# Kernel tuning notes

Hardware: AMD Instinct MI355X
Metric: run time of the kernel (lower is better)

## Reference

```python
import jax, jax.numpy as jnp
import numpy as np

MODEL_DIM = 1024
TOTAL_DIM = 1024
N_HEADS = 16
HEAD_DIM = TOTAL_DIM // N_HEADS


def setup_inputs() -> dict:
    key = jax.random.key(0)
    k1, k2, k3 = jax.random.split(key, 3)
    query = jax.random.normal(k1, (2, 2048, MODEL_DIM), dtype=jnp.float32)
    # nn.Linear(model_dim, 3*total_dim, bias=False): store as [in, out] for x @ W
    W_in = jax.random.normal(k2, (MODEL_DIM, 3 * TOTAL_DIM), dtype=jnp.float32) / np.sqrt(MODEL_DIM)
    W_out = jax.random.normal(k3, (TOTAL_DIM, MODEL_DIM), dtype=jnp.float32) / np.sqrt(TOTAL_DIM)
    return {"query": query, "W_in": W_in, "W_out": W_out}


def reference(query, W_in, W_out):
    B, S, _ = query.shape
    qkv = query @ W_in                      # [B, S, 3*D]
    q, k, v = jnp.split(qkv, 3, axis=-1)    # each [B, S, D]

    def to_heads(t):
        return t.reshape(B, S, N_HEADS, HEAD_DIM).transpose(0, 2, 1, 3)  # [B,H,S,d]

    q, k, v = to_heads(q), to_heads(k), to_heads(v)
    scale = 1.0 / np.sqrt(HEAD_DIM).astype(np.float32)
    scores = jnp.einsum('bhqd,bhkd->bhqk', q, k) * scale  # [B,H,S,S]
    causal = jnp.tril(jnp.ones((S, S), dtype=bool))
    scores = jnp.where(causal, scores, jnp.finfo(scores.dtype).min)
    probs = jax.nn.softmax(scores, axis=-1)
    attn = jnp.einsum('bhqk,bhkd->bhqd', probs, v)        # [B,H,S,d]
    attn = attn.transpose(0, 2, 1, 3).reshape(B, S, TOTAL_DIM)
    return attn @ W_out                     # [B, S, model_dim]
```

## Files before the change

### kernel.cpp

```cpp
#include <hip/hip_runtime.h>


typedef __bf16 bf16x8 __attribute__((ext_vector_type(8)));
typedef __bf16 bf16x4 __attribute__((ext_vector_type(4)));
typedef short s16x4 __attribute__((ext_vector_type(4)));
typedef float f32x4 __attribute__((ext_vector_type(4)));
typedef int i32x2 __attribute__((ext_vector_type(2)));

#define B_   2
#define S_   2048
#define DM   1024
#define NH   16
#define HD   64
#define N3   3072
#define M_   4096

#define SCALE_LOG2E 0.180336884f

__device__ __forceinline__ unsigned short f2bf(float f) {
  unsigned int u = __float_as_uint(f);
  u += 0x7fffu + ((u >> 16) & 1u);
  return (unsigned short)(u >> 16);
}

__device__ __forceinline__ void gload_lds16(void* lds, const void* g) {
  __builtin_amdgcn_global_load_lds(
      (__attribute__((address_space(1))) void*)g,
      (__attribute__((address_space(3))) void*)lds, 16, 0, 0);
}

__device__ __forceinline__ f32x4 mfma16(bf16x4 a, bf16x4 b, f32x4 c) {
#if __has_builtin(__builtin_amdgcn_mfma_f32_16x16x16_bf16)
  return __builtin_amdgcn_mfma_f32_16x16x16_bf16(a, b, c, 0, 0, 0);
#else
  return __builtin_amdgcn_mfma_f32_16x16x16bf16_1k(
      __builtin_bit_cast(s16x4, a), __builtin_bit_cast(s16x4, b), c, 0, 0, 0);
#endif
}

__device__ __forceinline__ int cvtpk(float s0, float s1) {
  int r;
  asm("v_cvt_pk_bf16_f32 %0, %1, %2" : "=v"(r) : "v"(s0), "v"(s1));
  return r;
}

__global__ __launch_bounds__(256) void prep(
    const float* __restrict__ query, const float* __restrict__ w_in,
    const float* __restrict__ w_out, unsigned short* __restrict__ qbf,
    unsigned short* __restrict__ w_in_t, unsigned short* __restrict__ w_out_t) {
  __shared__ float tile[32][33];
  const int bx = blockIdx.x;
  const int t = threadIdx.x;
  if (bx < 4096) {
    const int i = bx * 256 + t;
    const float4 v = ((const float4*)query)[i];
    ushort4 o;
    o.x = f2bf(v.x); o.y = f2bf(v.y); o.z = f2bf(v.z); o.w = f2bf(v.w);
    *(ushort4*)(&qbf[(size_t)i * 4]) = o;
    return;
  }
  const int tx = t & 31, ty = t >> 5;
  const float* in;
  unsigned short* out;
  int R, C, bxx, bxy, scale_rows;
  if (bx < 4096 + 3072) {
    const int id = bx - 4096;
    in = w_in; out = w_in_t; R = DM; C = N3;
    bxx = id % 96; bxy = id / 96; scale_rows = DM;
  } else {
    const int id = bx - 7168;
    in = w_out; out = w_out_t; R = DM; C = DM;
    bxx = id & 31; bxy = id >> 5; scale_rows = 0;
  }
  const int x = bxx * 32 + tx;
  const int y0 = bxy * 32;
#pragma unroll
  for (int j = 0; j < 32; j += 8)
    tile[ty + j][tx] = in[(size_t)(y0 + ty + j) * C + x];
  __syncthreads();
  const int ox = y0 + tx;
  const int oy0 = bxx * 32;
#pragma unroll
  for (int j = 0; j < 32; j += 8) {
    const int orow = oy0 + ty + j;
    float v = tile[tx][ty + j];
    if (orow < scale_rows) v *= SCALE_LOG2E;
    out[(size_t)orow * R + ox] = f2bf(v);
  }
}

__global__ __launch_bounds__(256) void gemm_qkv(
    const unsigned short* __restrict__ A, const unsigned short* __restrict__ Bt,
    unsigned short* __restrict__ qkv, unsigned short* __restrict__ vTn) {
  __shared__ __align__(16) unsigned short a_sm[128 * 32];
  __shared__ __align__(16) unsigned short b_sm[128 * 32];
  const int tid = threadIdx.x;
  const int lane = tid & 63, wave = tid >> 6;
  const int quad = lane >> 4, l15 = lane & 15;
  const int row0 = blockIdx.y * 128, col0 = blockIdx.x * 128;
  const int wm = (wave >> 1) * 64, wn = (wave & 1) * 64;
  const int K = DM;

  f32x4 acc[4][4];
#pragma unroll
  for (int i = 0; i < 4; i++)
#pragma unroll
    for (int j = 0; j < 4; j++) acc[i][j] = (f32x4){0.f, 0.f, 0.f, 0.f};

  const int e0 = tid * 8;

  for (int k0 = 0; k0 < K; k0 += 32) {
    __syncthreads();
#pragma unroll
    for (int i = 0; i < 2; i++) {
      int e = e0 + i * 2048;
      int r = e >> 5, c = e & 31;
      gload_lds16(&a_sm[e], &A[(size_t)(row0 + r) * K + k0 + c]);
      gload_lds16(&b_sm[e], &Bt[(size_t)(col0 + r) * K + k0 + c]);
    }
    __syncthreads();

    bf16x8 af[4], bfb[4];
#pragma unroll
    for (int i = 0; i < 4; i++) {
      af[i]  = *(const bf16x8*)&a_sm[(wm + i * 16 + l15) * 32 + quad * 8];
      bfb[i] = *(const bf16x8*)&b_sm[(wn + i * 16 + l15) * 32 + quad * 8];
    }
#pragma unroll
    for (int i = 0; i < 4; i++)
#pragma unroll
      for (int j = 0; j < 4; j++)
        acc[i][j] = __builtin_amdgcn_mfma_f32_16x16x32_bf16(af[i], bfb[j], acc[i][j], 0, 0, 0);
  }

  if (col0 + wn < 2 * DM) {
#pragma unroll
    for (int i = 0; i < 4; i++) {
#pragma unroll
      for (int j = 0; j < 4; j++) {
#pragma unroll
        for (int r = 0; r < 4; r++) {
          const int row = row0 + wm + i * 16 + quad * 4 + r;
          const int col = col0 + wn + j * 16 + l15;
          qkv[(size_t)row * N3 + col] = f2bf(acc[i][j][r]);
        }
      }
    }
  } else {
    const int head = (col0 + wn - 2 * DM) >> 6;
#pragma unroll
    for (int i = 0; i < 4; i++) {
      const int row = row0 + wm + i * 16 + quad * 4;
      const int b = row >> 11;
      const int srow = row & 2047;
      const int kt = srow >> 6;
      const int s = srow & 63;
      const int p = s >> 5, half = (s >> 4) & 1, q = (s >> 2) & 3;
      const size_t base = (size_t)((b * NH + head) * 32 + kt) * 4096;
#pragma unroll
      for (int j = 0; j < 4; j++) {
        const int d = j * 16 + l15;
        ushort4 w;
        w.x = f2bf(acc[i][j][0]);
        w.y = f2bf(acc[i][j][1]);
        w.z = f2bf(acc[i][j][2]);
        w.w = f2bf(acc[i][j][3]);
        *(ushort4*)&vTn[base + (size_t)(p * 256 + d * 4 + q) * 8 + half * 4] = w;
      }
    }
  }
}

__global__ __launch_bounds__(256) void gemm_abt_64(
    const unsigned short* __restrict__ A, const unsigned short* __restrict__ Bt,
    float* __restrict__ C, int M, int N, int K) {
  __shared__ __align__(16) unsigned short a_sm[64 * 32];
  __shared__ __align__(16) unsigned short b_sm[128 * 32];
  const int tid = threadIdx.x;
  const int lane = tid & 63, wave = tid >> 6;
  const int quad = lane >> 4, l15 = lane & 15;
  const int row0 = blockIdx.y * 64, col0 = blockIdx.x * 128;
  const int wn = wave * 32;

  f32x4 acc[4][2];
#pragma unroll
  for (int i = 0; i < 4; i++)
#pragma unroll
    for (int j = 0; j < 2; j++) acc[i][j] = (f32x4){0.f, 0.f, 0.f, 0.f};

  const int e0 = tid * 8;

  for (int k0 = 0; k0 < K; k0 += 32) {
    __syncthreads();
    {
      const int r = e0 >> 5, c = e0 & 31;
      gload_lds16(&a_sm[e0], &A[(size_t)(row0 + r) * K + k0 + c]);
    }
#pragma unroll
    for (int i = 0; i < 2; i++) {
      int e = e0 + i * 2048;
      int r = e >> 5, c = e & 31;
      gload_lds16(&b_sm[e], &Bt[(size_t)(col0 + r) * K + k0 + c]);
    }
    __syncthreads();

    bf16x8 af[4], bfb[2];
#pragma unroll
    for (int i = 0; i < 4; i++)
      af[i] = *(const bf16x8*)&a_sm[(i * 16 + l15) * 32 + quad * 8];
#pragma unroll
    for (int j = 0; j < 2; j++)
      bfb[j] = *(const bf16x8*)&b_sm[(wn + j * 16 + l15) * 32 + quad * 8];
#pragma unroll
    for (int i = 0; i < 4; i++)
#pragma unroll
      for (int j = 0; j < 2; j++)
        acc[i][j] = __builtin_amdgcn_mfma_f32_16x16x32_bf16(af[i], bfb[j], acc[i][j], 0, 0, 0);
  }

#pragma unroll
  for (int i = 0; i < 4; i++) {
#pragma unroll
    for (int j = 0; j < 2; j++) {
#pragma unroll
      for (int r = 0; r < 4; r++) {
        const int row = row0 + i * 16 + quad * 4 + r;
        const int col = col0 + wn + j * 16 + l15;
        C[(size_t)row * N + col] = acc[i][j][r];
      }
    }
  }
}

__global__ __launch_bounds__(512, 4) void attn_fused13(
    const unsigned short* __restrict__ qkv,
    const unsigned short* __restrict__ vTn,
    unsigned short* __restrict__ attnout) {
  const int p = blockIdx.x + (blockIdx.y << 4) + (blockIdx.z << 8);
  const int lg = ((p & 7) << 6) + (p >> 3);
  const int j = lg & 15;
  const int h = (lg >> 4) & 15;
  const int b = lg >> 8;

  const int tid = threadIdx.x;
  const int lane = tid & 63, wave = tid >> 6;
  const int quad = lane >> 4, l15 = lane & 15;
  const int sw = l15 & 7;

  __shared__ __align__(16) unsigned short k_sm[4 * 4096];
  __shared__ __align__(16) unsigned short vt_sm[4 * 4096];

  const int wrow0 = (wave < 4) ? (j * 64 + wave * 16)
                               : ((31 - j) * 64 + (wave - 4) * 16);
  const int qrow = wrow0 + l15;

  bf16x8 qf[2];
  {
    const unsigned short* qp = qkv + (size_t)(b * S_ + qrow) * N3 + h * HD + quad * 8;
    qf[0] = *(const bf16x8*)qp;
    qf[1] = *(const bf16x8*)(qp + 32);
  }

  f32x4 o[4];
#pragma unroll
  for (int n = 0; n < 4; n++) o[n] = (f32x4){0.f, 0.f, 0.f, 0.f};
  float lsum = 0.f;

  const int r0s = tid >> 3;
  const int gch = ((tid & 7) ^ (r0s & 7)) * 8;
  const unsigned short* kgb = qkv + (size_t)(b * S_ + r0s) * N3 + DM + h * HD + gch;
  const unsigned short* vgl = vTn + (size_t)((b * NH + h) * 32) * 4096 + tid * 8;

  const int nt = 32 - j;
  const int nR = (nt + 1) >> 1;

  auto STAGE = [&](int t) {
    const int bu = (t & 3) * 4096;
    gload_lds16(&k_sm[bu + tid * 8], kgb + (size_t)t * 64 * N3);
    gload_lds16(&vt_sm[bu + tid * 8], vgl + (size_t)t * 4096);
  };

  auto SUBTILE = [&](int t) {
    const unsigned short* kb = &k_sm[(t & 3) * 4096];
    const unsigned short* vb = &vt_sm[(t & 3) * 4096];

    f32x4 s[4];
#pragma unroll
    for (int mb = 0; mb < 4; mb++) s[mb] = (f32x4){0.f, 0.f, 0.f, 0.f};
    __builtin_amdgcn_s_setprio(1);
#pragma unroll
    for (int mb = 0; mb < 4; mb++) {
      const int ro = (mb * 16 + l15) * 64;
      bf16x8 kf0 = *(const bf16x8*)&kb[ro + ((quad ^ sw) << 3)];
      bf16x8 kf1 = *(const bf16x8*)&kb[ro + (((4 + quad) ^ sw) << 3)];
      s[mb] = __builtin_amdgcn_mfma_f32_16x16x32_bf16(kf0, qf[0], s[mb], 0, 0, 0);
      s[mb] = __builtin_amdgcn_mfma_f32_16x16x32_bf16(kf1, qf[1], s[mb], 0, 0, 0);
    }
    __builtin_amdgcn_s_setprio(0);

    if (t * 64 + 63 <= wrow0) {
#pragma unroll
      for (int mb = 0; mb < 4; mb++)
#pragma unroll
        for (int r = 0; r < 4; r++)
          s[mb][r] = exp2f(s[mb][r]);
    } else {
      const int kq0 = t * 64 + quad * 4;
#pragma unroll
      for (int mb = 0; mb < 4; mb++)
#pragma unroll
        for (int r = 0; r < 4; r++) {
          const float e = exp2f(s[mb][r]);
          s[mb][r] = (kq0 + mb * 16 + r <= qrow) ? e : 0.f;
        }
    }
#pragma unroll
    for (int mb = 0; mb < 4; mb++)
      lsum += (s[mb][0] + s[mb][1]) + (s[mb][2] + s[mb][3]);

    int pk[4][2];
#pragma unroll
    for (int mb = 0; mb < 4; mb++) {
      pk[mb][0] = cvtpk(s[mb][0], s[mb][1]);
      pk[mb][1] = cvtpk(s[mb][2], s[mb][3]);
    }

    __builtin_amdgcn_s_setprio(1);
#pragma unroll
    for (int pp = 0; pp < 2; pp++) {
      i32x2 wlo, whi;
      wlo.x = pk[2 * pp][0];     wlo.y = pk[2 * pp][1];
      whi.x = pk[2 * pp + 1][0]; whi.y = pk[2 * pp + 1][1];
      const bf16x4 blo = __builtin_bit_cast(bf16x4, wlo);
      const bf16x4 bhi = __builtin_bit_cast(bf16x4, whi);
#pragma unroll
      for (int mb = 0; mb < 4; mb++) {
        const bf16x8 vv =
            *(const bf16x8*)&vb[(pp * 256 + mb * 64 + l15 * 4 + quad) * 8];
        bf16x4 alo, ahi;
#pragma unroll
        for (int i = 0; i < 4; i++) { alo[i] = vv[i]; ahi[i] = vv[i + 4]; }
        o[mb] = mfma16(alo, blo, o[mb]);
        o[mb] = mfma16(ahi, bhi, o[mb]);
      }
    }
    __builtin_amdgcn_s_setprio(0);
  };

  STAGE(0);
  if (1 < nt) STAGE(1);

  for (int r = 0; r < nR; r++) {
    const int t0 = 2 * r, t1 = 2 * r + 1;
    asm volatile("s_waitcnt vmcnt(0)" ::: "memory");
    __builtin_amdgcn_s_barrier();
    __builtin_amdgcn_sched_barrier(0);
    if (r + 1 < nR) {
      STAGE(t0 + 2);
      if (t1 + 2 < nt) STAGE(t1 + 2);
    }
    if (t0 * 64 <= wrow0 + 15) SUBTILE(t0);
    if (t1 < nt && t1 * 64 <= wrow0 + 15) SUBTILE(t1);
  }

  asm volatile("s_waitcnt vmcnt(0)" ::: "memory");

  float l = lsum;
  l += __shfl_xor(l, 16);
  l += __shfl_xor(l, 32);
  const float inv = 1.0f / l;
  const size_t grow = (size_t)(b * S_ + qrow);
#pragma unroll
  for (int mb = 0; mb < 4; mb++) {
    ushort4 w;
    w.x = f2bf(o[mb][0] * inv);
    w.y = f2bf(o[mb][1] * inv);
    w.z = f2bf(o[mb][2] * inv);
    w.w = f2bf(o[mb][3] * inv);
    *(ushort4*)&attnout[grow * DM + h * HD + mb * 16 + quad * 4] = w;
  }
}

extern "C" void kernel_launch(void* const* d_in, const int* in_sizes, int n_in,
                              void* d_out, int out_size, void* d_ws, size_t ws_size,
                              hipStream_t stream) {
  const float* query = (const float*)d_in[0];
  const float* w_in  = (const float*)d_in[1];
  const float* w_out = (const float*)d_in[2];
  float* out = (float*)d_out;

  char* ws = (char*)d_ws;
  unsigned short* qbf     = (unsigned short*)(ws);
  unsigned short* attn    = (unsigned short*)(ws);
  unsigned short* w_in_t  = (unsigned short*)(ws + 8388608);
  unsigned short* w_out_t = (unsigned short*)(ws + 14680064);
  unsigned short* qkv     = (unsigned short*)(ws + 16777216);
  unsigned short* vTn     = (unsigned short*)(ws + 41943040);

  prep<<<dim3(8192), dim3(256), 0, stream>>>(query, w_in, w_out, qbf, w_in_t, w_out_t);
  gemm_qkv<<<dim3(N3 / 128, M_ / 128), dim3(256), 0, stream>>>(qbf, w_in_t, qkv, vTn);
  attn_fused13<<<dim3(16, NH, B_), dim3(512), 0, stream>>>(qkv, vTn, attn);
  gemm_abt_64<<<dim3(DM / 128, M_ / 64), dim3(256), 0, stream>>>(attn, w_out_t, out, M_, DM, DM);
}
```

Baseline: 189.4 us.

## Double-buffer LDS in QKV and output GEMMs to overlap loads with MFMA

Both projection GEMMs now keep two LDS buffers. The next K-tile is issued with direct global-to-LDS loads while MFMAs run on the current tile, and each iteration uses one barrier instead of two. Wave priority is raised around the MFMA block. This doubles LDS use per block, which may lower occupancy, and it relies on a manual vmcnt wait before each barrier being enough to order the LDS reads against the next overwrite.

After: 197.9 us. +4.5%, slower.

```diff
diff --git a/kernel.cpp b/kernel.cpp
--- a/kernel.cpp
+++ b/kernel.cpp
@@ -92,14 +92,15 @@
 __global__ __launch_bounds__(256) void gemm_qkv(
     const unsigned short* __restrict__ A, const unsigned short* __restrict__ Bt,
     unsigned short* __restrict__ qkv, unsigned short* __restrict__ vTn) {
-  __shared__ __align__(16) unsigned short a_sm[128 * 32];
-  __shared__ __align__(16) unsigned short b_sm[128 * 32];
+  __shared__ __align__(16) unsigned short a_sm[2][128 * 32];
+  __shared__ __align__(16) unsigned short b_sm[2][128 * 32];
   const int tid = threadIdx.x;
   const int lane = tid & 63, wave = tid >> 6;
   const int quad = lane >> 4, l15 = lane & 15;
   const int row0 = blockIdx.y * 128, col0 = blockIdx.x * 128;
   const int wm = (wave >> 1) * 64, wn = (wave & 1) * 64;
   const int K = DM;
+  const int NK = K / 32;
 
   f32x4 acc[4][4];
 #pragma unroll
@@ -109,28 +110,43 @@
 
   const int e0 = tid * 8;
 
-  for (int k0 = 0; k0 < K; k0 += 32) {
-    __syncthreads();
+  auto STAGE = [&](int kt, int bi) {
+    const int k0 = kt * 32;
 #pragma unroll
     for (int i = 0; i < 2; i++) {
       int e = e0 + i * 2048;
       int r = e >> 5, c = e & 31;
-      gload_lds16(&a_sm[e], &A[(size_t)(row0 + r) * K + k0 + c]);
-      gload_lds16(&b_sm[e], &Bt[(size_t)(col0 + r) * K + k0 + c]);
-    }
-    __syncthreads();
+      gload_lds16(&a_sm[bi][e], &A[(size_t)(row0 + r) * K + k0 + c]);
+      gload_lds16(&b_sm[bi][e], &Bt[(size_t)(col0 + r) * K + k0 + c]);
+    }
+  };
+
+  STAGE(0, 0);
+  asm volatile("s_waitcnt vmcnt(0)" ::: "memory");
+  __builtin_amdgcn_s_barrier();
+
+  for (int kt = 0; kt < NK; kt++) {
+    const int cur = kt & 1;
+    if (kt + 1 < NK) STAGE(kt + 1, cur ^ 1);
 
     bf16x8 af[4], bfb[4];
 #pragma unroll
     for (int i = 0; i < 4; i++) {
-      af[i]  = *(const bf16x8*)&a_sm[(wm + i * 16 + l15) * 32 + quad * 8];
-      bfb[i] = *(const bf16x8*)&b_sm[(wn + i * 16 + l15) * 32 + quad * 8];
-    }
+      af[i]  = *(const bf16x8*)&a_sm[cur][(wm + i * 16 + l15) * 32 + quad * 8];
+      bfb[i] = *(const bf16x8*)&b_sm[cur][(wn + i * 16 + l15) * 32 + quad * 8];
+    }
+    __builtin_amdgcn_s_setprio(1);
 #pragma unroll
     for (int i = 0; i < 4; i++)
 #pragma unroll
       for (int j = 0; j < 4; j++)
         acc[i][j] = __builtin_amdgcn_mfma_f32_16x16x32_bf16(af[i], bfb[j], acc[i][j], 0, 0, 0);
+    __builtin_amdgcn_s_setprio(0);
+
+    if (kt + 1 < NK) {
+      asm volatile("s_waitcnt vmcnt(0)" ::: "memory");
+      __builtin_amdgcn_s_barrier();
+    }
   }
 
   if (col0 + wn < 2 * DM) {
@@ -174,13 +190,14 @@
 __global__ __launch_bounds__(256) void gemm_abt_64(
     const unsigned short* __restrict__ A, const unsigned short* __restrict__ Bt,
     float* __restrict__ C, int M, int N, int K) {
-  __shared__ __align__(16) unsigned short a_sm[64 * 32];
-  __shared__ __align__(16) unsigned short b_sm[128 * 32];
+  __shared__ __align__(16) unsigned short a_sm[2][64 * 32];
+  __shared__ __align__(16) unsigned short b_sm[2][128 * 32];
   const int tid = threadIdx.x;
   const int lane = tid & 63, wave = tid >> 6;
   const int quad = lane >> 4, l15 = lane & 15;
   const int row0 = blockIdx.y * 64, col0 = blockIdx.x * 128;
   const int wn = wave * 32;
+  const int NK = K / 32;
 
   f32x4 acc[4][2];
 #pragma unroll
@@ -190,32 +207,47 @@
 
   const int e0 = tid * 8;
 
-  for (int k0 = 0; k0 < K; k0 += 32) {
-    __syncthreads();
+  auto STAGE = [&](int kt, int bi) {
+    const int k0 = kt * 32;
     {
       const int r = e0 >> 5, c = e0 & 31;
-      gload_lds16(&a_sm[e0], &A[(size_t)(row0 + r) * K + k0 + c]);
+      gload_lds16(&a_sm[bi][e0], &A[(size_t)(row0 + r) * K + k0 + c]);
     }
 #pragma unroll
     for (int i = 0; i < 2; i++) {
       int e = e0 + i * 2048;
       int r = e >> 5, c = e & 31;
-      gload_lds16(&b_sm[e], &Bt[(size_t)(col0 + r) * K + k0 + c]);
-    }
-    __syncthreads();
+      gload_lds16(&b_sm[bi][e], &Bt[(size_t)(col0 + r) * K + k0 + c]);
+    }
+  };
+
+  STAGE(0, 0);
+  asm volatile("s_waitcnt vmcnt(0)" ::: "memory");
+  __builtin_amdgcn_s_barrier();
+
+  for (int kt = 0; kt < NK; kt++) {
+    const int cur = kt & 1;
+    if (kt + 1 < NK) STAGE(kt + 1, cur ^ 1);
 
     bf16x8 af[4], bfb[2];
 #pragma unroll
     for (int i = 0; i < 4; i++)
-      af[i] = *(const bf16x8*)&a_sm[(i * 16 + l15) * 32 + quad * 8];
+      af[i] = *(const bf16x8*)&a_sm[cur][(i * 16 + l15) * 32 + quad * 8];
 #pragma unroll
     for (int j = 0; j < 2; j++)
-      bfb[j] = *(const bf16x8*)&b_sm[(wn + j * 16 + l15) * 32 + quad * 8];
+      bfb[j] = *(const bf16x8*)&b_sm[cur][(wn + j * 16 + l15) * 32 + quad * 8];
+    __builtin_amdgcn_s_setprio(1);
 #pragma unroll
     for (int i = 0; i < 4; i++)
 #pragma unroll
       for (int j = 0; j < 2; j++)
         acc[i][j] = __builtin_amdgcn_mfma_f32_16x16x32_bf16(af[i], bfb[j], acc[i][j], 0, 0, 0);
+    __builtin_amdgcn_s_setprio(0);
+
+    if (kt + 1 < NK) {
+      asm volatile("s_waitcnt vmcnt(0)" ::: "memory");
+      __builtin_amdgcn_s_barrier();
+    }
   }
 
 #pragma unroll
```
